# Performance work log

Hardware: AMD Instinct MI355X
Metric: run time of the kernel (lower is better)

## Reference

```python
import jax, jax.numpy as jnp
import numpy as np

N_NODES = 50000
N_EDGES = 800000
IN_F, OUT_F = 128, 128
NUM_HEADS, QUERY_DIM = 3, 8


def setup_inputs() -> dict:
    key = jax.random.key(0)
    ks = jax.random.split(key, 8)
    scale = 1.0 / np.sqrt(IN_F)
    return {
        "x": jax.random.normal(ks[0], (N_NODES, IN_F), dtype=jnp.float32),
        "adj": jax.random.randint(ks[1], (2, N_EDGES), 0, N_NODES, dtype=jnp.int64),
        "Wq": jax.random.normal(ks[2], (QUERY_DIM * NUM_HEADS, IN_F), dtype=jnp.float32) * scale,
        "bq": jax.random.normal(ks[3], (QUERY_DIM * NUM_HEADS,), dtype=jnp.float32) * 0.01,
        "aw": jax.random.normal(ks[4], (NUM_HEADS, 2 * QUERY_DIM * NUM_HEADS), dtype=jnp.float32) * 0.1,
        "ab": jax.random.normal(ks[5], (NUM_HEADS,), dtype=jnp.float32) * 0.01,
        "lw": jax.random.normal(ks[6], (OUT_F, IN_F), dtype=jnp.float32) * scale,
        "lb": jax.random.normal(ks[7], (OUT_F,), dtype=jnp.float32) * 0.01,
    }


def reference(x, adj, Wq, bq, aw, ab, lw, lb):
    n = x.shape[0]
    s, r = adj[0], adj[1]
    # per-node query features: [N, H*Q]
    attr = x @ Wq.T + bq
    # per-edge attention logits from concat(sender, receiver): [E, H]
    e = jnp.concatenate((attr[s], attr[r]), axis=1) @ aw.T + ab
    # segment softmax over incoming edges of each receiver
    seg_max = jax.ops.segment_max(e, r, num_segments=n)  # [N, H]
    e = jnp.exp(e - jax.lax.stop_gradient(seg_max)[r])
    denom = jax.ops.segment_sum(e, r, num_segments=n)  # [N, H]
    alpha = e / jnp.maximum(denom[r], 1e-16)  # [E, H]
    # node value projection and attention-weighted aggregation
    h = x @ lw.T + lb  # [N, OUT_F]
    msg = h[s] * alpha.mean(axis=1, keepdims=True)  # [E, OUT_F]
    out = jax.ops.segment_sum(msg, r, num_segments=n)  # [N, OUT_F]
    return jax.nn.silu(out)
```

## Files before the change

### kernel.cpp

```cpp
#include <hip/hip_runtime.h>
#include <hip/hip_fp16.h>
#include <math.h>

#define N_NODES 50000
#define N_EDGES 800000
#define IN_F 128
#define OUT_F 128
#define NH 3
#define SCAN_NB ((N_NODES + 255) / 256)
#define NODE_NB ((N_NODES + 31) / 32)
#define NBH 32
#define EPB (N_EDGES / NBH)
#define QNODES (N_NODES / 4)
#define CQ_BLOCKS (NBH * 4)

typedef __attribute__((ext_vector_type(8))) _Float16 f16x8;
typedef __attribute__((ext_vector_type(4))) float f32x4;

__global__ __launch_bounds__(256) void weights_kernel(
    const float* __restrict__ Wq, const float* __restrict__ bq,
    const float* __restrict__ aw, const float* __restrict__ ab,
    const float* __restrict__ lw,
    _Float16* __restrict__ w2h, float* __restrict__ b2,
    _Float16* __restrict__ lwh)
{
    int t = blockIdx.x * 256 + threadIdx.x;
    if (t < 16 * 128) {
        int prow = t >> 7;
        int i    = t & 127;
        int r = -1;
        if (prow < 3) r = prow;
        else if (prow >= 4 && prow < 7) r = prow - 1;
        if (r < 0) {
            w2h[prow * 128 + i] = (_Float16)0.0f;
        } else {
            int hh  = (r < 3) ? r : r - 3;
            int off = (r < 3) ? 0 : 24;
            const float* awr = aw + hh * 48 + off;
            float acc = 0.0f;
            #pragma unroll
            for (int q = 0; q < 24; q++) acc += awr[q] * Wq[q * 128 + i];
            w2h[prow * 128 + i] = (_Float16)acc;
            if (i == 0) {
                float b = 0.0f;
                #pragma unroll
                for (int q = 0; q < 24; q++) b += awr[q] * bq[q];
                if (r >= 3) b += ab[hh];
                b2[r] = b;
            }
        }
    }
    int u = t - 16 * 128;
    if (u >= 0 && u < 128 * 128) lwh[u] = (_Float16)lw[u];
}

__global__ __launch_bounds__(256) void node_count_kernel(
    const float* __restrict__ x, const _Float16* __restrict__ lwh,
    const float* __restrict__ lb, const _Float16* __restrict__ w2h,
    const float* __restrict__ b2, const int* __restrict__ adj,
    __half* __restrict__ h, float* __restrict__ as4, float* __restrict__ ar4,
    unsigned int* __restrict__ hist, unsigned short* __restrict__ rank)
{
    __shared__ __align__(16) unsigned int shmem[QNODES / 2];

    if (blockIdx.x < CQ_BLOCKS) {
        unsigned int* cnt = shmem;
        for (int i = threadIdx.x; i < QNODES / 2; i += 256) cnt[i] = 0;
        __syncthreads();
        const int c = blockIdx.x >> 2, q = blockIdx.x & 3;
        const int nlo = q * QNODES;
        const int e0 = c * EPB, e1 = e0 + EPB;
        for (int base = e0 + threadIdx.x; base < e1; base += 8 * 256) {
            int rs[8];
            #pragma unroll
            for (int u = 0; u < 8; u++) {
                int e = base + u * 256;
                rs[u] = (e < e1) ? adj[N_EDGES + e] : -1;
            }
            #pragma unroll
            for (int u = 0; u < 8; u++) {
                int e = base + u * 256;
                int lr = rs[u] - nlo;
                if ((unsigned)lr < (unsigned)QNODES) {
                    int sh = (lr & 1) * 16;
                    unsigned int old = atomicAdd(&cnt[lr >> 1], 1u << sh);
                    rank[e] = (unsigned short)(old >> sh);
                }
            }
        }
        __syncthreads();
        unsigned int* hb = hist + (size_t)c * (N_NODES / 2) + q * (QNODES / 2);
        for (int i = threadIdx.x; i < QNODES / 2; i += 256)
            hb[i] = cnt[i];
        return;
    }

    unsigned char* xs = (unsigned char*)shmem;
    const int tx = threadIdx.x;
    const int nb = (blockIdx.x - CQ_BLOCKS) * 32;

    #pragma unroll
    for (int it = 0; it < 2; it++) {
        int cc = it * 256 + tx;
        int node = cc >> 4, kc = cc & 15;
        int gn = nb + node;
        f16x8 v;
        if (gn < N_NODES) {
            const float4* xr = (const float4*)(x + (size_t)gn * 128 + kc * 8);
            float4 p = xr[0], qq = xr[1];
            v[0] = (_Float16)p.x;  v[1] = (_Float16)p.y;
            v[2] = (_Float16)p.z;  v[3] = (_Float16)p.w;
            v[4] = (_Float16)qq.x; v[5] = (_Float16)qq.y;
            v[6] = (_Float16)qq.z; v[7] = (_Float16)qq.w;
        } else {
            #pragma unroll
            for (int e = 0; e < 8; e++) v[e] = (_Float16)0.0f;
        }
        int byte = node * 256 + ((kc * 16) ^ ((node & 7) << 4));
        *(f16x8*)(xs + byte) = v;
    }
    __syncthreads();

    const int wave = tx >> 6, lane = tx & 63;
    const int l15 = lane & 15, lg = lane >> 4;

    f16x8 afr[2][4];
    #pragma unroll
    for (int m = 0; m < 2; m++) {
        int out = wave * 32 + m * 16 + l15;
        const f16x8* ar8 = (const f16x8*)(lwh + (size_t)out * 128);
        #pragma unroll
        for (int kk = 0; kk < 4; kk++)
            afr[m][kk] = ar8[kk * 4 + lg];
    }
    f16x8 a6[4];
    {
        const f16x8* w8 = (const f16x8*)(w2h + (size_t)l15 * 128);
        #pragma unroll
        for (int kk = 0; kk < 4; kk++) a6[kk] = w8[kk * 4 + lg];
    }

    f32x4 acc[2][2], acc6[2];
    #pragma unroll
    for (int m = 0; m < 2; m++)
        #pragma unroll
        for (int n = 0; n < 2; n++)
            acc[m][n] = (f32x4){0.f, 0.f, 0.f, 0.f};
    #pragma unroll
    for (int n = 0; n < 2; n++) acc6[n] = (f32x4){0.f, 0.f, 0.f, 0.f};

    #pragma unroll
    for (int kk = 0; kk < 4; kk++) {
        f16x8 bfr[2];
        #pragma unroll
        for (int n = 0; n < 2; n++) {
            int node = n * 16 + l15;
            int byte = node * 256 + ((kk * 64 + lg * 16) ^ ((node & 7) << 4));
            bfr[n] = *(const f16x8*)(xs + byte);
        }
        #pragma unroll
        for (int m = 0; m < 2; m++)
            #pragma unroll
            for (int n = 0; n < 2; n++)
                acc[m][n] = __builtin_amdgcn_mfma_f32_16x16x32_f16(
                    afr[m][kk], bfr[n], acc[m][n], 0, 0, 0);
        if (wave == 0) {
            #pragma unroll
            for (int n = 0; n < 2; n++)
                acc6[n] = __builtin_amdgcn_mfma_f32_16x16x32_f16(
                    a6[kk], bfr[n], acc6[n], 0, 0, 0);
        }
    }

    #pragma unroll
    for (int n = 0; n < 2; n++) {
        int gn = nb + n * 16 + l15;
        if (gn >= N_NODES) continue;
        #pragma unroll
        for (int m = 0; m < 2; m++) {
            int outb = wave * 32 + m * 16 + lg * 4;
            float4 lbv = *(const float4*)&lb[outb];
            __half2 p0 = __floats2half2_rn(acc[m][n].x + lbv.x, acc[m][n].y + lbv.y);
            __half2 p1 = __floats2half2_rn(acc[m][n].z + lbv.z, acc[m][n].w + lbv.w);
            int2 st;
            st.x = *(int*)&p0;
            st.y = *(int*)&p1;
            *(int2*)&h[(size_t)gn * 128 + outb] = st;
        }
    }

    if (wave == 0 && lg < 2) {
        float b0, bx, by;
        if (lg == 0) { b0 = b2[0]; bx = b2[1]; by = b2[2]; }
        else         { b0 = b2[3]; bx = b2[4]; by = b2[5]; }
        #pragma unroll
        for (int n = 0; n < 2; n++) {
            int gn = nb + n * 16 + l15;
            if (gn >= N_NODES) continue;
            float4 v = make_float4(acc6[n].x + b0, acc6[n].y + bx,
                                   acc6[n].z + by, 0.0f);
            if (lg == 0) *(float4*)&as4[(size_t)gn * 4] = v;
            else         *(float4*)&ar4[(size_t)gn * 4] = v;
        }
    }
}

__global__ __launch_bounds__(256) void scan_kernel(
    const unsigned int* __restrict__ hist, int* __restrict__ start,
    unsigned short* __restrict__ offs16,
    int* __restrict__ psum, int* __restrict__ poffs, int* __restrict__ sync)
{
    const int t = threadIdx.x, b = blockIdx.x;
    const int i = b * 256 + t;
    const int w = i >> 1, sh = (i & 1) * 16;
    int tot = 0;
    if (i < N_NODES) {
        for (int c = 0; c < NBH; c++)
            tot += (hist[(size_t)c * (N_NODES / 2) + w] >> sh) & 0xffff;
    }
    __shared__ int shm[256];
    shm[t] = tot;
    __syncthreads();
    #pragma unroll
    for (int off = 1; off < 256; off <<= 1) {
        int u = (t >= off) ? shm[t - off] : 0;
        __syncthreads();
        shm[t] += u;
        __syncthreads();
    }
    const int incl = shm[t];
    if (t == 255)
        __hip_atomic_store(&psum[b], incl, __ATOMIC_RELAXED,
                           __HIP_MEMORY_SCOPE_AGENT);
    __syncthreads();
    if (t == 0)
        __hip_atomic_fetch_add(&sync[0], 1, __ATOMIC_RELEASE,
                               __HIP_MEMORY_SCOPE_AGENT);

    if (b == 0) {
        if (t == 0)
            while (__hip_atomic_load(&sync[0], __ATOMIC_ACQUIRE,
                                     __HIP_MEMORY_SCOPE_AGENT) < SCAN_NB) {}
        __syncthreads();
        int pv = (t < SCAN_NB)
               ? __hip_atomic_load(&psum[t], __ATOMIC_RELAXED,
                                   __HIP_MEMORY_SCOPE_AGENT)
               : 0;
        shm[t] = pv;
        __syncthreads();
        #pragma unroll
        for (int off = 1; off < 256; off <<= 1) {
            int u = (t >= off) ? shm[t - off] : 0;
            __syncthreads();
            shm[t] += u;
            __syncthreads();
        }
        if (t < SCAN_NB)
            __hip_atomic_store(&poffs[t], shm[t] - pv, __ATOMIC_RELAXED,
                               __HIP_MEMORY_SCOPE_AGENT);
        __syncthreads();
        if (t == 0)
            __hip_atomic_store(&sync[1], 1, __ATOMIC_RELEASE,
                               __HIP_MEMORY_SCOPE_AGENT);
    }

    if (t == 0)
        while (__hip_atomic_load(&sync[1], __ATOMIC_ACQUIRE,
                                 __HIP_MEMORY_SCOPE_AGENT) == 0) {}
    __syncthreads();
    const int base = __hip_atomic_load(&poffs[b], __ATOMIC_RELAXED,
                                       __HIP_MEMORY_SCOPE_AGENT);
    if (i < N_NODES) {
        start[i] = base + incl - tot;
        int acc = 0;
        for (int c = 0; c < NBH; c++) {
            offs16[(size_t)c * N_NODES + i] = (unsigned short)acc;
            acc += (hist[(size_t)c * (N_NODES / 2) + w] >> sh) & 0xffff;
        }
    }
    if (i == N_NODES - 1) start[N_NODES] = base + incl;
}

__global__ __launch_bounds__(256) void fill_kernel(
    const int* __restrict__ adj, const int* __restrict__ start,
    const unsigned short* __restrict__ offs16,
    const unsigned short* __restrict__ rank,
    unsigned short* __restrict__ srcs)
{
    int e = blockIdx.x * 512 + threadIdx.x;
    #pragma unroll
    for (int u = 0; u < 2; u++, e += 256) {
        if (e < N_EDGES) {
            int r = adj[N_EDGES + e];
            int cb = e / EPB;
            int pos = start[r] + (int)offs16[(size_t)cb * N_NODES + r]
                    + (int)rank[e];
            srcs[pos] = (unsigned short)adj[e];
        }
    }
}

__global__ __launch_bounds__(256) void agg_kernel(
    const int* __restrict__ start, const unsigned short* __restrict__ srcs,
    const float4* __restrict__ as4, const float* __restrict__ ar4,
    const __half* __restrict__ h, float* __restrict__ out)
{
    const int wave = threadIdx.x >> 6;
    const int lane = threadIdx.x & 63;
    const int n = blockIdx.x * 4 + wave;
    if (n >= N_NODES) return;
    const int s0 = start[n], s1 = start[n + 1];
    const int deg = s1 - s0;

    __shared__ float sh_c[4][65];
    __shared__ int   sh_s[4][65];

    const float4 cr = *(const float4*)&ar4[(size_t)n * 4];
    const int half = lane >> 5, sub = lane & 31;
    const int2* hq = (const int2*)h;
    float a0 = 0.f, a1 = 0.f, a2 = 0.f, a3 = 0.f;

    if (deg <= 64) {
        float e0 = 0.f, e1 = 0.f, e2 = 0.f;
        int s = 0;
        if (lane < deg) {
            s = srcs[s0 + lane];
            float4 a = as4[s];
            e0 = __expf(a.x + cr.x);
            e1 = __expf(a.y + cr.y);
            e2 = __expf(a.z + cr.z);
        }
        float p0 = e0, p1 = e1, p2 = e2;
        #pragma unroll
        for (int off = 32; off >= 1; off >>= 1) {
            p0 += __shfl_xor(p0, off);
            p1 += __shfl_xor(p1, off);
            p2 += __shfl_xor(p2, off);
        }
        const float i0 = (1.0f / 3.0f) / fmaxf(p0, 1e-30f);
        const float i1 = (1.0f / 3.0f) / fmaxf(p1, 1e-30f);
        const float i2 = (1.0f / 3.0f) / fmaxf(p2, 1e-30f);
        if (lane < deg) {
            sh_s[wave][lane] = s;
            sh_c[wave][lane] = e0 * i0 + e1 * i1 + e2 * i2;
        } else if (lane == deg) {
            sh_s[wave][lane] = 0;
            sh_c[wave][lane] = 0.0f;
        }
        #pragma unroll 4
        for (int j = 0; j < deg; j += 2) {
            int jj = j + half;
            float c = sh_c[wave][jj];
            int sj = sh_s[wave][jj];
            int2 hv = hq[(size_t)sj * 32 + sub];
            float2 f0 = __half22float2(*(const __half2*)&hv.x);
            float2 f1 = __half22float2(*(const __half2*)&hv.y);
            a0 += c * f0.x; a1 += c * f0.y;
            a2 += c * f1.x; a3 += c * f1.y;
        }
    } else {
        float p0 = 0.f, p1 = 0.f, p2 = 0.f;
        for (int k = s0 + lane; k < s1; k += 64) {
            float4 a = as4[srcs[k]];
            p0 += __expf(a.x + cr.x);
            p1 += __expf(a.y + cr.y);
            p2 += __expf(a.z + cr.z);
        }
        #pragma unroll
        for (int off = 32; off >= 1; off >>= 1) {
            p0 += __shfl_xor(p0, off);
            p1 += __shfl_xor(p1, off);
            p2 += __shfl_xor(p2, off);
        }
        const float i0 = (1.0f / 3.0f) / fmaxf(p0, 1e-30f);
        const float i1 = (1.0f / 3.0f) / fmaxf(p1, 1e-30f);
        const float i2 = (1.0f / 3.0f) / fmaxf(p2, 1e-30f);

        for (int cb = s0; cb < s1; cb += 64) {
            int cnt = min(64, s1 - cb);
            if (lane < cnt) {
                int s = srcs[cb + lane];
                float4 a = as4[s];
                sh_s[wave][lane] = s;
                sh_c[wave][lane] = __expf(a.x + cr.x) * i0
                                 + __expf(a.y + cr.y) * i1
                                 + __expf(a.z + cr.z) * i2;
            } else if (lane == cnt) {
                sh_s[wave][lane] = 0;
                sh_c[wave][lane] = 0.0f;
            }
            #pragma unroll 4
            for (int j = 0; j < cnt; j += 2) {
                int jj = j + half;
                float c = sh_c[wave][jj];
                int sj = sh_s[wave][jj];
                int2 hv = hq[(size_t)sj * 32 + sub];
                float2 f0 = __half22float2(*(const __half2*)&hv.x);
                float2 f1 = __half22float2(*(const __half2*)&hv.y);
                a0 += c * f0.x; a1 += c * f0.y;
                a2 += c * f1.x; a3 += c * f1.y;
            }
        }
    }

    a0 += __shfl_xor(a0, 32);
    a1 += __shfl_xor(a1, 32);
    a2 += __shfl_xor(a2, 32);
    a3 += __shfl_xor(a3, 32);
    if (half == 0) {
        float4 o;
        o.x = a0 / (1.0f + __expf(-a0));
        o.y = a1 / (1.0f + __expf(-a1));
        o.z = a2 / (1.0f + __expf(-a2));
        o.w = a3 / (1.0f + __expf(-a3));
        *(float4*)&out[(size_t)n * 128 + sub * 4] = o;
    }
}

extern "C" void kernel_launch(void* const* d_in, const int* in_sizes, int n_in,
                              void* d_out, int out_size, void* d_ws, size_t ws_size,
                              hipStream_t stream)
{
    const float* x  = (const float*)d_in[0];
    const int*   adj= (const int*)  d_in[1];
    const float* Wq = (const float*)d_in[2];
    const float* bq = (const float*)d_in[3];
    const float* aw = (const float*)d_in[4];
    const float* ab = (const float*)d_in[5];
    const float* lw = (const float*)d_in[6];
    const float* lb = (const float*)d_in[7];
    float* out = (float*)d_out;

    _Float16* w2h = (_Float16*)d_ws;
    float* b2     = (float*)(w2h + 2048);
    _Float16* lwh = (_Float16*)(b2 + 8);
    float* as4    = (float*)(lwh + 16384);
    float* ar4    = as4 + (size_t)N_NODES * 4;
    __half* h     = (__half*)(ar4 + (size_t)N_NODES * 4);
    int* start    = (int*)(h + (size_t)N_NODES * 128);
    int* sync     = start + (N_NODES + 1);
    unsigned int* hist = (unsigned int*)(sync + 8);
    unsigned short* offs16 = (unsigned short*)(hist + (size_t)NBH * (N_NODES / 2));
    unsigned short* rank   = offs16 + (size_t)NBH * N_NODES;
    unsigned short* srcs   = rank + N_EDGES;
    int* psum     = (int*)(srcs + N_EDGES);
    int* poffs    = psum + 256;

    hipMemsetAsync(sync, 0, 8 * sizeof(int), stream);

    weights_kernel<<<72, 256, 0, stream>>>(Wq, bq, aw, ab, lw, w2h, b2, lwh);

    node_count_kernel<<<CQ_BLOCKS + NODE_NB, 256, 0, stream>>>(
        x, lwh, lb, w2h, b2, adj, h, as4, ar4, hist, rank);

    scan_kernel<<<SCAN_NB, 256, 0, stream>>>(hist, start, offs16,
                                             psum, poffs, sync);

    fill_kernel<<<(N_EDGES + 511) / 512, 256, 0, stream>>>(
        adj, start, offs16, rank, srcs);

    agg_kernel<<<(N_NODES + 3) / 4, 256, 0, stream>>>(
        start, srcs, (const float4*)as4, ar4, h, out);
}
```

Measured before the change: 120.7 us.

## Split aggregation into coefficient pass and column-sliced SpMM over sliced h layout

Stores h in 8 column slices of 16 halves per node, so each slice (50000 nodes × 32 bytes) is a small contiguous array that can stay cache-resident. The fused softmax+aggregate kernel is split into a coef_kernel that writes (src, coefficient) pairs per edge and an spmm_kernel where each block handles one slice for 32 nodes. The aim is better L2 locality for the random gathers. The cost is an extra kernel launch, an extra 6.4 MB round trip for the edge coefficients, and each edge list being re-read once per slice.

```diff
diff --git a/kernel.cpp b/kernel.cpp
--- a/kernel.cpp
+++ b/kernel.cpp
@@ -13,9 +13,13 @@
 #define EPB (N_EDGES / NBH)
 #define QNODES (N_NODES / 4)
 #define CQ_BLOCKS (NBH * 4)
+#define NSLICE 8
+#define SLICE_HALVES (N_NODES * 16)
 
 typedef __attribute__((ext_vector_type(8))) _Float16 f16x8;
 typedef __attribute__((ext_vector_type(4))) float f32x4;
+typedef __attribute__((ext_vector_type(2))) float f32x2;
+typedef __attribute__((ext_vector_type(2))) int i32x2;
 
 __global__ __launch_bounds__(256) void weights_kernel(
     const float* __restrict__ Wq, const float* __restrict__ bq,
@@ -185,7 +189,9 @@
             int2 st;
             st.x = *(int*)&p0;
             st.y = *(int*)&p1;
-            *(int2*)&h[(size_t)gn * 128 + outb] = st;
+            int slice = outb >> 4;
+            int col   = outb & 15;
+            *(int2*)&h[(size_t)slice * SLICE_HALVES + (size_t)gn * 16 + col] = st;
         }
     }
 
@@ -300,10 +306,10 @@
     }
 }
 
-__global__ __launch_bounds__(256) void agg_kernel(
+__global__ __launch_bounds__(256) void coef_kernel(
     const int* __restrict__ start, const unsigned short* __restrict__ srcs,
     const float4* __restrict__ as4, const float* __restrict__ ar4,
-    const __half* __restrict__ h, float* __restrict__ out)
+    i32x2* __restrict__ ec)
 {
     const int wave = threadIdx.x >> 6;
     const int lane = threadIdx.x & 63;
@@ -311,14 +317,7 @@
     if (n >= N_NODES) return;
     const int s0 = start[n], s1 = start[n + 1];
     const int deg = s1 - s0;
-
-    __shared__ float sh_c[4][65];
-    __shared__ int   sh_s[4][65];
-
     const float4 cr = *(const float4*)&ar4[(size_t)n * 4];
-    const int half = lane >> 5, sub = lane & 31;
-    const int2* hq = (const int2*)h;
-    float a0 = 0.f, a1 = 0.f, a2 = 0.f, a3 = 0.f;
 
     if (deg <= 64) {
         float e0 = 0.f, e1 = 0.f, e2 = 0.f;
@@ -341,22 +340,10 @@
         const float i1 = (1.0f / 3.0f) / fmaxf(p1, 1e-30f);
         const float i2 = (1.0f / 3.0f) / fmaxf(p2, 1e-30f);
         if (lane < deg) {
-            sh_s[wave][lane] = s;
-            sh_c[wave][lane] = e0 * i0 + e1 * i1 + e2 * i2;
-        } else if (lane == deg) {
-            sh_s[wave][lane] = 0;
-            sh_c[wave][lane] = 0.0f;
-        }
-        #pragma unroll 4
-        for (int j = 0; j < deg; j += 2) {
-            int jj = j + half;
-            float c = sh_c[wave][jj];
-            int sj = sh_s[wave][jj];
-            int2 hv = hq[(size_t)sj * 32 + sub];
-            float2 f0 = __half22float2(*(const __half2*)&hv.x);
-            float2 f1 = __half22float2(*(const __half2*)&hv.y);
-            a0 += c * f0.x; a1 += c * f0.y;
-            a2 += c * f1.x; a3 += c * f1.y;
+            i32x2 v;
+            v.x = s;
+            v.y = __float_as_int(e0 * i0 + e1 * i1 + e2 * i2);
+            ec[s0 + lane] = v;
         }
     } else {
         float p0 = 0.f, p1 = 0.f, p2 = 0.f;
@@ -375,45 +362,69 @@
         const float i0 = (1.0f / 3.0f) / fmaxf(p0, 1e-30f);
         const float i1 = (1.0f / 3.0f) / fmaxf(p1, 1e-30f);
         const float i2 = (1.0f / 3.0f) / fmaxf(p2, 1e-30f);
-
-        for (int cb = s0; cb < s1; cb += 64) {
-            int cnt = min(64, s1 - cb);
-            if (lane < cnt) {
-                int s = srcs[cb + lane];
-                float4 a = as4[s];
-                sh_s[wave][lane] = s;
-                sh_c[wave][lane] = __expf(a.x + cr.x) * i0
-                                 + __expf(a.y + cr.y) * i1
-                                 + __expf(a.z + cr.z) * i2;
-            } else if (lane == cnt) {
-                sh_s[wave][lane] = 0;
-                sh_c[wave][lane] = 0.0f;
-            }
-            #pragma unroll 4
-            for (int j = 0; j < cnt; j += 2) {
-                int jj = j + half;
-                float c = sh_c[wave][jj];
-                int sj = sh_s[wave][jj];
-                int2 hv = hq[(size_t)sj * 32 + sub];
-                float2 f0 = __half22float2(*(const __half2*)&hv.x);
-                float2 f1 = __half22float2(*(const __half2*)&hv.y);
-                a0 += c * f0.x; a1 += c * f0.y;
-                a2 += c * f1.x; a3 += c * f1.y;
-            }
-        }
-    }
-
-    a0 += __shfl_xor(a0, 32);
-    a1 += __shfl_xor(a1, 32);
-    a2 += __shfl_xor(a2, 32);
-    a3 += __shfl_xor(a3, 32);
-    if (half == 0) {
-        float4 o;
+        for (int k = s0 + lane; k < s1; k += 64) {
+            int s = srcs[k];
+            float4 a = as4[s];
+            i32x2 v;
+            v.x = s;
+            v.y = __float_as_int(__expf(a.x + cr.x) * i0
+                               + __expf(a.y + cr.y) * i1
+                               + __expf(a.z + cr.z) * i2);
+            ec[k] = v;
+        }
+    }
+}
+
+__global__ __launch_bounds__(256) void spmm_kernel(
+    const int* __restrict__ start, const i32x2* __restrict__ ec,
+    const __half* __restrict__ h, float* __restrict__ out)
+{
+    const int slice = blockIdx.x & 7;
+    const int tile  = blockIdx.x >> 3;
+    const int col2  = threadIdx.x & 7;
+    const int nsub  = threadIdx.x >> 3;
+    const int n = tile * 32 + nsub;
+    const __half2* hsl = (const __half2*)(h + (size_t)slice * SLICE_HALVES);
+
+    int s0 = 0, s1 = 0;
+    if (n < N_NODES) { s0 = start[n]; s1 = start[n + 1]; }
+    float a0 = 0.f, a1 = 0.f;
+
+    int k = s0;
+    for (; k + 4 <= s1; k += 4) {
+        i32x2 E0 = __builtin_nontemporal_load(&ec[k]);
+        i32x2 E1 = __builtin_nontemporal_load(&ec[k + 1]);
+        i32x2 E2 = __builtin_nontemporal_load(&ec[k + 2]);
+        i32x2 E3 = __builtin_nontemporal_load(&ec[k + 3]);
+        __half2 h0 = hsl[(unsigned)E0.x * 8u + col2];
+        __half2 h1 = hsl[(unsigned)E1.x * 8u + col2];
+        __half2 h2 = hsl[(unsigned)E2.x * 8u + col2];
+        __half2 h3 = hsl[(unsigned)E3.x * 8u + col2];
+        float c0 = __int_as_float(E0.y), c1 = __int_as_float(E1.y);
+        float c2 = __int_as_float(E2.y), c3 = __int_as_float(E3.y);
+        a0 = fmaf(__half2float(h0.x), c0, a0);
+        a1 = fmaf(__half2float(h0.y), c0, a1);
+        a0 = fmaf(__half2float(h1.x), c1, a0);
+        a1 = fmaf(__half2float(h1.y), c1, a1);
+        a0 = fmaf(__half2float(h2.x), c2, a0);
+        a1 = fmaf(__half2float(h2.y), c2, a1);
+        a0 = fmaf(__half2float(h3.x), c3, a0);
+        a1 = fmaf(__half2float(h3.y), c3, a1);
+    }
+    for (; k < s1; ++k) {
+        i32x2 E = __builtin_nontemporal_load(&ec[k]);
+        __half2 hv = hsl[(unsigned)E.x * 8u + col2];
+        float c = __int_as_float(E.y);
+        a0 = fmaf(__half2float(hv.x), c, a0);
+        a1 = fmaf(__half2float(hv.y), c, a1);
+    }
+
+    if (n < N_NODES) {
+        f32x2 o;
         o.x = a0 / (1.0f + __expf(-a0));
         o.y = a1 / (1.0f + __expf(-a1));
-        o.z = a2 / (1.0f + __expf(-a2));
-        o.w = a3 / (1.0f + __expf(-a3));
-        *(float4*)&out[(size_t)n * 128 + sub * 4] = o;
+        __builtin_nontemporal_store(
+            o, (f32x2*)(out + (size_t)n * 128 + slice * 16 + col2 * 2));
     }
 }
 
@@ -437,7 +448,8 @@
     float* as4    = (float*)(lwh + 16384);
     float* ar4    = as4 + (size_t)N_NODES * 4;
     __half* h     = (__half*)(ar4 + (size_t)N_NODES * 4);
-    int* start    = (int*)(h + (size_t)N_NODES * 128);
+    i32x2* ec     = (i32x2*)(h + (size_t)N_NODES * 128);
+    int* start    = (int*)(ec + N_EDGES);
     int* sync     = start + (N_NODES + 1);
     unsigned int* hist = (unsigned int*)(sync + 8);
     unsigned short* offs16 = (unsigned short*)(hist + (size_t)NBH * (N_NODES / 2));
@@ -459,6 +471,9 @@
     fill_kernel<<<(N_EDGES + 511) / 512, 256, 0, stream>>>(
         adj, start, offs16, rank, srcs);
 
-    agg_kernel<<<(N_NODES + 3) / 4, 256, 0, stream>>>(
-        start, srcs, (const float4*)as4, ar4, h, out);
-}
+    coef_kernel<<<(N_NODES + 3) / 4, 256, 0, stream>>>(
+        start, srcs, (const float4*)as4, ar4, ec);
+
+    spmm_kernel<<<NSLICE * ((N_NODES + 31) / 32), 256, 0, stream>>>(
+        start, ec, h, out);
+}
```

New measurement: 193.0 us. 1.6x slower.
